# Kernel tuning notes

Hardware: AMD Instinct MI355X
Metric: run time of the kernel (lower is better)

The kernel has to match this reference:

```python
import jax, jax.numpy as jnp
import numpy as np

N_NODES = 100000
N_EDGES = 1000000
F_IN = 32       # CFG.feature_dim
H = 64          # CFG.hidden_dim
H2 = 2 * H      # L1 family: conv1 out = hidden_dim * 2
N_GRAPHS = 64


def gcn_conv(x, src, dst, deg_inv_sqrt, W, b, num_nodes):
    # PyG GCNConv: out = D^{-1/2} (A + I) D^{-1/2} (x @ W) + b
    h = x @ W  # [N, out]
    norm = (deg_inv_sqrt[src] * deg_inv_sqrt[dst])[:, None]  # [E+N, 1]
    msg = h[src] * norm
    return jax.ops.segment_sum(msg, dst, num_segments=num_nodes) + b


def setup_inputs() -> dict:
    key = jax.random.key(0)
    ks = jax.random.split(key, 10)
    x = jax.random.normal(ks[0], (N_NODES, F_IN), dtype=jnp.float32)
    edge_index = jax.random.randint(ks[1], (2, N_EDGES), 0, N_NODES, dtype=jnp.int64)
    batch = jnp.sort(jax.random.randint(ks[2], (N_NODES,), 0, N_GRAPHS, dtype=jnp.int64))
    def glorot(k, shape):
        lim = np.sqrt(6.0 / (shape[0] + shape[1]))
        return jax.random.uniform(k, shape, jnp.float32, -lim, lim)
    W1 = glorot(ks[3], (F_IN, H2))
    b1 = jnp.zeros((H2,), jnp.float32)
    W2 = glorot(ks[4], (H2, H))
    b2 = jnp.zeros((H,), jnp.float32)
    Wrt = glorot(ks[5], (H, H))
    brt = jnp.zeros((H,), jnp.float32)
    return {"x": x, "edge_index": edge_index, "batch": batch,
            "W1": W1, "b1": b1, "W2": W2, "b2": b2, "Wrt": Wrt, "brt": brt}


def reference(x, edge_index, batch, W1, b1, W2, b2, Wrt, brt):
    num_nodes = x.shape[0]
    loop = jnp.arange(num_nodes, dtype=edge_index.dtype)
    src = jnp.concatenate([edge_index[0], loop])  # add self-loops
    dst = jnp.concatenate([edge_index[1], loop])
    deg = jax.ops.segment_sum(jnp.ones_like(dst, dtype=x.dtype), dst, num_segments=num_nodes)
    deg_inv_sqrt = jnp.where(deg > 0, jax.lax.rsqrt(deg), 0.0)

    h = jax.nn.relu(gcn_conv(x, src, dst, deg_inv_sqrt, W1, b1, num_nodes))
    h = gcn_conv(h, src, dst, deg_inv_sqrt, W2, b2, num_nodes)
    h = h @ Wrt + brt  # L1 reverse transcriptase

    # global_mean_pool over batch segments
    sums = jax.ops.segment_sum(h, batch, num_segments=N_GRAPHS)
    counts = jax.ops.segment_sum(jnp.ones((num_nodes,), h.dtype), batch, num_segments=N_GRAPHS)
    pooled = sums / jnp.maximum(counts, 1.0)[:, None]

    activity_factor = 1.0  # age = 0 -> 1/(1+0)
    return pooled * activity_factor
```

## Files before the change

### kernel.cpp

```cpp
#include <hip/hip_runtime.h>

#define NN 100000
#define NE 1000000
#define FIN 32
#define H2 128
#define HH 64
#define NG 64
#define SLOT 16
#define OSLOT 48

#define BSH 9
#define BNODES 512
#define NB 196
#define CAPL 28
#define CAPB 6144
#define CHUNK 2048
#define NSPILL 4096

typedef __attribute__((ext_vector_type(8))) short short8;
typedef __attribute__((ext_vector_type(4))) float f32x4;
typedef __attribute__((ext_vector_type(2))) float f32x2;

__device__ __forceinline__ unsigned f2bf(float f) {
    unsigned u = __float_as_uint(f);
    return (u + 0x7FFFu + ((u >> 16) & 1u)) >> 16;
}
__device__ __forceinline__ float bf2f(unsigned u) {
    return __uint_as_float(u << 16);
}
__device__ __forceinline__ void acc8(float* a, float w, uint4 v) {
    a[0] = fmaf(w, bf2f(v.x & 0xFFFFu), a[0]);
    a[1] = fmaf(w, bf2f(v.x >> 16), a[1]);
    a[2] = fmaf(w, bf2f(v.y & 0xFFFFu), a[2]);
    a[3] = fmaf(w, bf2f(v.y >> 16), a[3]);
    a[4] = fmaf(w, bf2f(v.z & 0xFFFFu), a[4]);
    a[5] = fmaf(w, bf2f(v.z >> 16), a[5]);
    a[6] = fmaf(w, bf2f(v.w & 0xFFFFu), a[6]);
    a[7] = fmaf(w, bf2f(v.w >> 16), a[7]);
}
__device__ __forceinline__ void dec8(float* a, float w, uint2 v) {
    f32x2 p0 = __builtin_amdgcn_cvt_pk_f32_fp8((int)v.x, false);
    f32x2 p1 = __builtin_amdgcn_cvt_pk_f32_fp8((int)v.x, true);
    f32x2 p2 = __builtin_amdgcn_cvt_pk_f32_fp8((int)v.y, false);
    f32x2 p3 = __builtin_amdgcn_cvt_pk_f32_fp8((int)v.y, true);
    a[0] = fmaf(w, p0.x, a[0]); a[1] = fmaf(w, p0.y, a[1]);
    a[2] = fmaf(w, p1.x, a[2]); a[3] = fmaf(w, p1.y, a[3]);
    a[4] = fmaf(w, p2.x, a[4]); a[5] = fmaf(w, p2.y, a[5]);
    a[6] = fmaf(w, p3.x, a[6]); a[7] = fmaf(w, p3.y, a[7]);
}
__device__ __forceinline__ unsigned char f2fp8(float f) {
    return (unsigned char)(__builtin_amdgcn_cvt_pk_fp8_f32(f, f, 0, false) & 0xff);
}


__global__ void k_zero(int* __restrict__ p, int n) {
    int i = blockIdx.x * 256 + threadIdx.x;
    if (i < n) p[i] = 0;
}

__global__ void k_cvtx(const float* __restrict__ x, uint4* __restrict__ xb) {
    int i = blockIdx.x * 256 + threadIdx.x;
    if (i >= NN * FIN / 8) return;
    float4 a = ((const float4*)x)[2 * i];
    float4 b = ((const float4*)x)[2 * i + 1];
    uint4 r;
    r.x = f2bf(a.x) | (f2bf(a.y) << 16);
    r.y = f2bf(a.z) | (f2bf(a.w) << 16);
    r.z = f2bf(b.x) | (f2bf(b.y) << 16);
    r.w = f2bf(b.z) | (f2bf(b.w) << 16);
    xb[i] = r;
}

__global__ void k_fold(const float* __restrict__ W2, const float* __restrict__ Wrt,
                       const float* __restrict__ b2, const float* __restrict__ brt,
                       const float* __restrict__ W1,
                       unsigned short* __restrict__ w2t, float* __restrict__ brt2,
                       unsigned short* __restrict__ w1t) {
    int i = blockIdx.x * 256 + threadIdx.x;
    if (i < H2 * HH) {
        int r = i >> 6, c = i & 63;
        float acc = 0.f;
        for (int k = 0; k < HH; ++k) acc = fmaf(W2[r * HH + k], Wrt[k * HH + c], acc);
        w2t[c * H2 + r] = (unsigned short)f2bf(acc);
    } else if (i < H2 * HH + HH) {
        int c = i - H2 * HH;
        float acc = brt[c];
        for (int k = 0; k < HH; ++k) acc = fmaf(b2[k], Wrt[k * HH + c], acc);
        brt2[c] = acc;
    } else if (i < H2 * HH + HH + FIN * H2) {
        int j = i - (H2 * HH + HH);
        int k = j >> 7, c = j & 127;
        w1t[c * FIN + k] = (unsigned short)f2bf(W1[j]);
    }
}

__global__ __launch_bounds__(256) void k_bin(const int* __restrict__ ei,
                                             int* __restrict__ gcnt,
                                             unsigned* __restrict__ gbuf,
                                             int* __restrict__ gspillc,
                                             int* __restrict__ gspill) {
    __shared__ int cur[NB];
    __shared__ int gbase[NB];
    __shared__ unsigned stage[NB * CAPL];
    for (int i = threadIdx.x; i < NB; i += 256) cur[i] = 0;
    __syncthreads();
    int e0 = blockIdx.x * CHUNK;
#pragma unroll
    for (int it = 0; it < CHUNK / 256; ++it) {
        int e = e0 + it * 256 + threadIdx.x;
        if (e < NE) {
            int d = ei[NE + e];
            int b = d >> BSH;
            unsigned u = ((unsigned)ei[e] << BSH) | (unsigned)(d & (BNODES - 1));
            int p = atomicAdd(&cur[b], 1);
            if (p < CAPL) stage[b * CAPL + p] = u;
            else {
                int q = atomicAdd(gspillc, 1);
                if (q < NSPILL) { gspill[2 * q] = b; gspill[2 * q + 1] = (int)u; }
            }
        }
    }
    __syncthreads();
    if (threadIdx.x < NB) {
        int len = min(cur[threadIdx.x], CAPL);
        gbase[threadIdx.x] = len ? atomicAdd(&gcnt[threadIdx.x], len) : 0;
    }
    __syncthreads();
    int wid = threadIdx.x >> 6, lane = threadIdx.x & 63;
    for (int b = wid; b < NB; b += 4) {
        int len = min(cur[b], CAPL);
        if (len == 0) continue;
        int base = gbase[b];
        if (base + len > CAPB) len = max(0, CAPB - base);
        if (lane < len)
            gbuf[(size_t)b * CAPB + base + lane] = stage[b * CAPL + lane];
    }
}

__global__ __launch_bounds__(512) void k_build(const unsigned* __restrict__ gbuf,
                                               const int* __restrict__ gcnt,
                                               const int* __restrict__ gspillc,
                                               const int* __restrict__ gspill,
                                               int* __restrict__ esrc,
                                               int* __restrict__ ovf,
                                               int* __restrict__ fill) {
    __shared__ int cnt[BNODES];
    __shared__ int slots[BNODES * SLOT];
    for (int i = threadIdx.x; i < BNODES; i += 512) cnt[i] = 0;
    __syncthreads();
    int b = blockIdx.x;
    int len = min(gcnt[b], CAPB);
    const unsigned* buf = gbuf + (size_t)b * CAPB;
    for (int i = threadIdx.x; i < len; i += 512) {
        unsigned u = buf[i];
        int ln = u & (BNODES - 1);
        int src = (int)(u >> BSH);
        int p = atomicAdd(&cnt[ln], 1);
        if (p < SLOT) slots[ln * SLOT + p] = src;
        else if (p < SLOT + OSLOT)
            ovf[(size_t)(b * BNODES + ln) * OSLOT + (p - SLOT)] = src;
    }
    int ns = min(*gspillc, NSPILL);
    for (int i = threadIdx.x; i < ns; i += 512) {
        if (gspill[2 * i] == b) {
            unsigned u = (unsigned)gspill[2 * i + 1];
            int ln = u & (BNODES - 1);
            int src = (int)(u >> BSH);
            int p = atomicAdd(&cnt[ln], 1);
            if (p < SLOT) slots[ln * SLOT + p] = src;
            else if (p < SLOT + OSLOT)
                ovf[(size_t)(b * BNODES + ln) * OSLOT + (p - SLOT)] = src;
        }
    }
    __syncthreads();
    int nbase = b * BNODES;
    int nvalid = min(BNODES, NN - nbase);
    if (nvalid <= 0) return;
    for (int i = threadIdx.x; i < nvalid; i += 512) fill[nbase + i] = cnt[i];
    int nwords = nvalid * SLOT / 4;
    int4* d4 = (int4*)(esrc + (size_t)nbase * SLOT);
    const int4* s4 = (const int4*)slots;
    for (int i = threadIdx.x; i < nwords; i += 512) d4[i] = s4[i];
}

__global__ void k_node(const int* __restrict__ cnt, const int* __restrict__ bat,
                       float* __restrict__ dis, int* __restrict__ counts) {
    int n = blockIdx.x * 256 + threadIdx.x;
    int lane = threadIdx.x & 63;
    if (n < NN) dis[n] = rsqrtf((float)(cnt[n] + 1));
    int g = (n < NN) ? bat[n] : -1;
    int gprev = __shfl_up(g, 1, 64);
    bool head = (lane == 0) || (g != gprev);
    unsigned long long hm = __ballot(head && (n < NN));
    int gnext = __shfl_down(g, 1, 64);
    bool tail = (n < NN) && ((lane == 63) || (gnext != g));
    if (tail) {
        unsigned long long below =
            (lane == 63) ? ~0ull : ((1ull << (lane + 1)) - 1ull);
        int start = 63 - __clzll(hm & below);
        atomicAdd(&counts[g], lane - start + 1);
    }
}

__global__ void k_pack(const int* __restrict__ cnt, const float* __restrict__ dis,
                       int* __restrict__ esrc, int* __restrict__ ovf) {
    int i = blockIdx.x * 256 + threadIdx.x;
    if (i >= NN * 64) return;
    int n = i >> 6, p = i & 63;
    int c = cnt[n];
    if (p < SLOT) {
        if (p >= min(c, SLOT)) return;
        int s = esrc[n * SLOT + p];
        esrc[n * SLOT + p] = (int)(((unsigned)s << 15) | (f2bf(dis[s]) & 0x7FFFu));
    } else {
        int q = p - SLOT;
        if (q >= min(c - SLOT, OSLOT)) return;
        int s = ovf[n * OSLOT + q];
        ovf[n * OSLOT + q] = (int)(((unsigned)s << 15) | (f2bf(dis[s]) & 0x7FFFu));
    }
}

__global__ __launch_bounds__(256, 4) void k_aggx(
    const uint4* __restrict__ xb4, const float* __restrict__ dis,
    const int* __restrict__ cnt, const int* __restrict__ esrc,
    const int* __restrict__ ovf, uint4* __restrict__ aggx4) {
    int idx = blockIdx.x * 256 + threadIdx.x;
    int n = idx >> 2, t = idx & 3;
    if (n >= NN) return;
    float dn = dis[n];
    float a[8];
    {
        uint4 xv = xb4[n * 4 + t];
        float s = dn * dn;
        a[0] = s * bf2f(xv.x & 0xFFFFu); a[1] = s * bf2f(xv.x >> 16);
        a[2] = s * bf2f(xv.y & 0xFFFFu); a[3] = s * bf2f(xv.y >> 16);
        a[4] = s * bf2f(xv.z & 0xFFFFu); a[5] = s * bf2f(xv.z >> 16);
        a[6] = s * bf2f(xv.w & 0xFFFFu); a[7] = s * bf2f(xv.w >> 16);
    }
    int c = cnt[n];
    int c1 = min(c, SLOT);
    if (c1 > 0) {
        const int4* rp = (const int4*)(esrc + (size_t)n * SLOT);
        int4 i0 = rp[0], i1 = rp[1], i2 = rp[2], i3 = rp[3];
        int ej[16] = {i0.x, i0.y, i0.z, i0.w, i1.x, i1.y, i1.z, i1.w,
                      i2.x, i2.y, i2.z, i2.w, i3.x, i3.y, i3.z, i3.w};
        int e0 = i0.x;
#pragma unroll
        for (int j = 0; j < 16; ++j) {
            int e = (j < c1) ? ej[j] : e0;
            int s = (int)((unsigned)e >> 15);
            float w = (j < c1) ? bf2f(e & 0x7FFF) * dn : 0.f;
            acc8(a, w, xb4[(size_t)s * 4 + t]);
        }
    }
    if (c > SLOT) {
        int cov = min(c - SLOT, OSLOT);
        const int* orow = ovf + (size_t)n * OSLOT;
        for (int p = 0; p < cov; ++p) {
            int e = orow[p];
            int s = (int)((unsigned)e >> 15);
            acc8(a, bf2f(e & 0x7FFF) * dn, xb4[(size_t)s * 4 + t]);
        }
    }
    uint4 r;
    r.x = f2bf(a[0]) | (f2bf(a[1]) << 16);
    r.y = f2bf(a[2]) | (f2bf(a[3]) << 16);
    r.z = f2bf(a[4]) | (f2bf(a[5]) << 16);
    r.w = f2bf(a[6]) | (f2bf(a[7]) << 16);
    aggx4[n * 4 + t] = r;
}

__global__ __launch_bounds__(256) void k_mlpm(
    const unsigned short* __restrict__ aggxg, const unsigned short* __restrict__ w1tg,
    const unsigned short* __restrict__ w2tg, const float* __restrict__ b1,
    unsigned char* __restrict__ y) {
    __shared__ unsigned short w1t[H2 * FIN];
    __shared__ unsigned short w2t[HH * H2];
    __shared__ float b1s[H2];
    __shared__ float h1s[4][16 * 132];
    for (int i = threadIdx.x; i < FIN * H2 / 8; i += 256)
        ((uint4*)w1t)[i] = ((const uint4*)w1tg)[i];
    for (int i = threadIdx.x; i < HH * H2 / 8; i += 256)
        ((uint4*)w2t)[i] = ((const uint4*)w2tg)[i];
    if (threadIdx.x < H2) b1s[threadIdx.x] = b1[threadIdx.x];
    __syncthreads();
    int wid = threadIdx.x >> 6, l = threadIdx.x & 63;
    int base = (blockIdx.x * 4 + wid) * 16;
    if (base >= NN) return;
    int lr = l & 15, lk = l >> 4;
    float* h1w = h1s[wid];
    const f32x4 zero = {0.f, 0.f, 0.f, 0.f};

    short8 a1 = ((const short8*)aggxg)[(base + lr) * 4 + lk];
#pragma unroll
    for (int ct = 0; ct < 8; ++ct) {
        short8 bf = *(const short8*)&w1t[(ct * 16 + lr) * FIN + lk * 8];
        f32x4 c = __builtin_amdgcn_mfma_f32_16x16x32_bf16(a1, bf, zero, 0, 0, 0);
        float bv = b1s[ct * 16 + lr];
#pragma unroll
        for (int q = 0; q < 4; ++q)
            h1w[(lk * 4 + q) * 132 + ct * 16 + lr] = fmaxf(c[q] + bv, 0.f);
    }

    f32x4 acc0 = zero, acc1 = zero, acc2 = zero, acc3 = zero;
#pragma unroll
    for (int kt = 0; kt < 4; ++kt) {
        const float* ap = &h1w[lr * 132 + kt * 32 + lk * 8];
        float4 alo = *(const float4*)ap;
        float4 ahi = *(const float4*)(ap + 4);
        short8 af;
        af[0] = (short)f2bf(alo.x); af[1] = (short)f2bf(alo.y);
        af[2] = (short)f2bf(alo.z); af[3] = (short)f2bf(alo.w);
        af[4] = (short)f2bf(ahi.x); af[5] = (short)f2bf(ahi.y);
        af[6] = (short)f2bf(ahi.z); af[7] = (short)f2bf(ahi.w);
        const unsigned short* wb = &w2t[lr * H2 + kt * 32 + lk * 8];
        short8 b0 = *(const short8*)(wb);
        short8 b1f = *(const short8*)(wb + 16 * H2);
        short8 b2f = *(const short8*)(wb + 32 * H2);
        short8 b3f = *(const short8*)(wb + 48 * H2);
        acc0 = __builtin_amdgcn_mfma_f32_16x16x32_bf16(af, b0, acc0, 0, 0, 0);
        acc1 = __builtin_amdgcn_mfma_f32_16x16x32_bf16(af, b1f, acc1, 0, 0, 0);
        acc2 = __builtin_amdgcn_mfma_f32_16x16x32_bf16(af, b2f, acc2, 0, 0, 0);
        acc3 = __builtin_amdgcn_mfma_f32_16x16x32_bf16(af, b3f, acc3, 0, 0, 0);
    }
    unsigned char* ybs = (unsigned char*)h1w;
#pragma unroll
    for (int q = 0; q < 4; ++q) {
        int r = lk * 4 + q;
        ybs[r * 64 + lr +  0] = f2fp8(acc0[q]);
        ybs[r * 64 + lr + 16] = f2fp8(acc1[q]);
        ybs[r * 64 + lr + 32] = f2fp8(acc2[q]);
        ybs[r * 64 + lr + 48] = f2fp8(acc3[q]);
    }
    ((uint4*)(y + (size_t)base * 64))[l] = ((const uint4*)ybs)[l];
}

__global__ __launch_bounds__(256, 4) void k_l2g(
    const uint2* __restrict__ y2, const float* __restrict__ dis,
    const int* __restrict__ cnt, const int* __restrict__ esrc,
    const int* __restrict__ ovf, const float* __restrict__ brt2,
    const int* __restrict__ bat, float* __restrict__ pool) {
    __shared__ float hred[32][HH];
    __shared__ int gids[32];
    int idx = blockIdx.x * 256 + threadIdx.x;
    int n = idx >> 3;
    int t = threadIdx.x & 7;
    int ni = threadIdx.x >> 3;
    float dn = dis[n];
    float a[8];
    {
        float4 blo = ((const float4*)brt2)[t * 2];
        float4 bhi = ((const float4*)brt2)[t * 2 + 1];
        a[0] = blo.x; a[1] = blo.y; a[2] = blo.z; a[3] = blo.w;
        a[4] = bhi.x; a[5] = bhi.y; a[6] = bhi.z; a[7] = bhi.w;
        dec8(a, dn * dn, y2[(size_t)n * 8 + t]);
    }
    int c = cnt[n];
    int c1 = min(c, SLOT);
    if (c1 > 0) {
        const int4* rp = (const int4*)(esrc + (size_t)n * SLOT);
        int4 i0 = rp[0], i1 = rp[1], i2 = rp[2], i3 = rp[3];
        int ej[16] = {i0.x, i0.y, i0.z, i0.w, i1.x, i1.y, i1.z, i1.w,
                      i2.x, i2.y, i2.z, i2.w, i3.x, i3.y, i3.z, i3.w};
        int e0 = i0.x;
#pragma unroll
        for (int j = 0; j < 16; ++j) {
            int e = (j < c1) ? ej[j] : e0;
            int s = (int)((unsigned)e >> 15);
            float w = (j < c1) ? bf2f(e & 0x7FFF) * dn : 0.f;
            dec8(a, w, y2[(size_t)s * 8 + t]);
        }
    }
    if (c > SLOT) {
        int cov = min(c - SLOT, OSLOT);
        const int* orow = ovf + (size_t)n * OSLOT;
        for (int p = 0; p < cov; ++p) {
            int e = orow[p];
            int s = (int)((unsigned)e >> 15);
            dec8(a, bf2f(e & 0x7FFF) * dn, y2[(size_t)s * 8 + t]);
        }
    }
    ((float4*)&hred[ni][t * 8])[0] = make_float4(a[0], a[1], a[2], a[3]);
    ((float4*)&hred[ni][t * 8])[1] = make_float4(a[4], a[5], a[6], a[7]);
    if (t == 0) gids[ni] = bat[n];
    __syncthreads();
    if (threadIdx.x < HH) {
        int f = threadIdx.x;
        int cg = gids[0];
        float s = 0.f;
        for (int j = 0; j < 32; ++j) {
            int g = gids[j];
            if (g != cg) { atomicAdd(&pool[cg * HH + f], s); s = 0.f; cg = g; }
            s += hred[j][f];
        }
        atomicAdd(&pool[cg * HH + f], s);
    }
}

__global__ void k_final(const float* __restrict__ pool, const int* __restrict__ counts,
                        float* __restrict__ out) {
    int i = blockIdx.x * 256 + threadIdx.x;
    if (i < NG * HH) {
        int g = i >> 6;
        out[i] = pool[i] / fmaxf((float)counts[g], 1.0f);
    }
}


extern "C" void kernel_launch(void* const* d_in, const int* in_sizes, int n_in,
                              void* d_out, int out_size, void* d_ws, size_t ws_size,
                              hipStream_t stream) {
    const float* x   = (const float*)d_in[0];
    const int*   ei  = (const int*)d_in[1];
    const int*   bat = (const int*)d_in[2];
    const float* W1  = (const float*)d_in[3];
    const float* b1  = (const float*)d_in[4];
    const float* W2  = (const float*)d_in[5];
    const float* b2  = (const float*)d_in[6];
    const float* Wrt = (const float*)d_in[7];
    const float* brt = (const float*)d_in[8];
    float* out = (float*)d_out;

    int* ws = (int*)d_ws;
    int* fill    = ws;
    int* counts  = ws + NN;
    float* pool  = (float*)(ws + NN + NG);
    int* gcnt    = ws + NN + NG + NG * HH;
    int* gspillc = gcnt + 256;
    const int ZN = NN + NG + NG * HH + 256 + 64;
    int* gspill  = ws + ZN;
    float* dis   = (float*)(gspill + 2 * NSPILL);
    int* esrc    = (int*)dis + NN;
    int* ovf     = esrc + (size_t)NN * SLOT;
    unsigned* gbuf = (unsigned*)(ovf + (size_t)NN * OSLOT);
    unsigned* xb   = (unsigned*)(gbuf + (size_t)NB * CAPB);
    unsigned* aggx = xb + NN * 16;
    unsigned char* yb = (unsigned char*)(aggx + NN * 16);
    unsigned short* w1t = (unsigned short*)(yb + (size_t)NN * 64);
    unsigned short* w2t = w1t + FIN * H2;
    float* brt2 = (float*)(w2t + H2 * HH);

    k_zero<<<(ZN + 255) / 256, 256, 0, stream>>>(ws, ZN);
    k_cvtx<<<(NN * FIN / 8 + 255) / 256, 256, 0, stream>>>(x, (uint4*)xb);
    k_fold<<<(H2 * HH + HH + FIN * H2 + 255) / 256, 256, 0, stream>>>(
        W2, Wrt, b2, brt, W1, w2t, brt2, w1t);
    k_bin<<<(NE + CHUNK - 1) / CHUNK, 256, 0, stream>>>(ei, gcnt, gbuf, gspillc, gspill);
    k_build<<<NB, 512, 0, stream>>>(gbuf, gcnt, gspillc, gspill, esrc, ovf, fill);
    k_node<<<(NN + 255) / 256, 256, 0, stream>>>(fill, bat, dis, counts);
    k_pack<<<(NN * 64 + 255) / 256, 256, 0, stream>>>(fill, dis, esrc, ovf);
    k_aggx<<<(NN * 4 + 255) / 256, 256, 0, stream>>>(
        (const uint4*)xb, dis, fill, esrc, ovf, (uint4*)aggx);
    k_mlpm<<<(NN + 63) / 64, 256, 0, stream>>>(
        (const unsigned short*)aggx, w1t, w2t, b1, yb);
    k_l2g<<<NN * 8 / 256, 256, 0, stream>>>(
        (const uint2*)yb, dis, fill, esrc, ovf, brt2, bat, pool);
    k_final<<<(NG * HH + 255) / 256, 256, 0, stream>>>(pool, counts, out);
}
```

Measured before the change: 120.7 us.

## Store input features as fp8 and merge setup kernels into one launch

The bf16 copy of x is replaced by an fp8 copy, which halves the bytes fetched per neighbor in the layer-one gather. Aggregation decodes it with the hardware fp8 conversion instructions. The zero, convert and weight-fold kernels are merged into a single setup kernel, removing two launches. The cost is lower input precision, which could push the result past the accuracy tolerance.

```diff
diff --git a/kernel.cpp b/kernel.cpp
--- a/kernel.cpp
+++ b/kernel.cpp
@@ -16,6 +16,7 @@
 #define CAPB 6144
 #define CHUNK 2048
 #define NSPILL 4096
+#define ZN (NN + NG + NG * HH + 256 + 64)
 
 typedef __attribute__((ext_vector_type(8))) short short8;
 typedef __attribute__((ext_vector_type(4))) float f32x4;
@@ -27,16 +28,6 @@
 }
 __device__ __forceinline__ float bf2f(unsigned u) {
     return __uint_as_float(u << 16);
-}
-__device__ __forceinline__ void acc8(float* a, float w, uint4 v) {
-    a[0] = fmaf(w, bf2f(v.x & 0xFFFFu), a[0]);
-    a[1] = fmaf(w, bf2f(v.x >> 16), a[1]);
-    a[2] = fmaf(w, bf2f(v.y & 0xFFFFu), a[2]);
-    a[3] = fmaf(w, bf2f(v.y >> 16), a[3]);
-    a[4] = fmaf(w, bf2f(v.z & 0xFFFFu), a[4]);
-    a[5] = fmaf(w, bf2f(v.z >> 16), a[5]);
-    a[6] = fmaf(w, bf2f(v.w & 0xFFFFu), a[6]);
-    a[7] = fmaf(w, bf2f(v.w >> 16), a[7]);
 }
 __device__ __forceinline__ void dec8(float* a, float w, uint2 v) {
     f32x2 p0 = __builtin_amdgcn_cvt_pk_f32_fp8((int)v.x, false);
@@ -52,31 +43,23 @@
     return (unsigned char)(__builtin_amdgcn_cvt_pk_fp8_f32(f, f, 0, false) & 0xff);
 }
 
-
-__global__ void k_zero(int* __restrict__ p, int n) {
+__global__ void k_setup(const float* __restrict__ x, const float* __restrict__ W1,
+                        const float* __restrict__ W2, const float* __restrict__ Wrt,
+                        const float* __restrict__ b2, const float* __restrict__ brt,
+                        int* __restrict__ zws, uint2* __restrict__ xb8,
+                        unsigned short* __restrict__ w2t, float* __restrict__ brt2,
+                        unsigned short* __restrict__ w1t) {
     int i = blockIdx.x * 256 + threadIdx.x;
-    if (i < n) p[i] = 0;
-}
-
-__global__ void k_cvtx(const float* __restrict__ x, uint4* __restrict__ xb) {
-    int i = blockIdx.x * 256 + threadIdx.x;
-    if (i >= NN * FIN / 8) return;
-    float4 a = ((const float4*)x)[2 * i];
-    float4 b = ((const float4*)x)[2 * i + 1];
-    uint4 r;
-    r.x = f2bf(a.x) | (f2bf(a.y) << 16);
-    r.y = f2bf(a.z) | (f2bf(a.w) << 16);
-    r.z = f2bf(b.x) | (f2bf(b.y) << 16);
-    r.w = f2bf(b.z) | (f2bf(b.w) << 16);
-    xb[i] = r;
-}
-
-__global__ void k_fold(const float* __restrict__ W2, const float* __restrict__ Wrt,
-                       const float* __restrict__ b2, const float* __restrict__ brt,
-                       const float* __restrict__ W1,
-                       unsigned short* __restrict__ w2t, float* __restrict__ brt2,
-                       unsigned short* __restrict__ w1t) {
-    int i = blockIdx.x * 256 + threadIdx.x;
+    if (i < ZN) zws[i] = 0;
+    if (i < NN * FIN / 8) {
+        float4 a = ((const float4*)x)[2 * i];
+        float4 b = ((const float4*)x)[2 * i + 1];
+        unsigned u0 = __builtin_amdgcn_cvt_pk_fp8_f32(a.x, a.y, 0, false);
+        u0 = __builtin_amdgcn_cvt_pk_fp8_f32(a.z, a.w, u0, true);
+        unsigned u1 = __builtin_amdgcn_cvt_pk_fp8_f32(b.x, b.y, 0, false);
+        u1 = __builtin_amdgcn_cvt_pk_fp8_f32(b.z, b.w, u1, true);
+        xb8[i] = make_uint2(u0, u1);
+    }
     if (i < H2 * HH) {
         int r = i >> 6, c = i & 63;
         float acc = 0.f;
@@ -221,22 +204,15 @@
 }
 
 __global__ __launch_bounds__(256, 4) void k_aggx(
-    const uint4* __restrict__ xb4, const float* __restrict__ dis,
+    const uint2* __restrict__ xb8, const float* __restrict__ dis,
     const int* __restrict__ cnt, const int* __restrict__ esrc,
     const int* __restrict__ ovf, uint4* __restrict__ aggx4) {
     int idx = blockIdx.x * 256 + threadIdx.x;
     int n = idx >> 2, t = idx & 3;
     if (n >= NN) return;
     float dn = dis[n];
-    float a[8];
-    {
-        uint4 xv = xb4[n * 4 + t];
-        float s = dn * dn;
-        a[0] = s * bf2f(xv.x & 0xFFFFu); a[1] = s * bf2f(xv.x >> 16);
-        a[2] = s * bf2f(xv.y & 0xFFFFu); a[3] = s * bf2f(xv.y >> 16);
-        a[4] = s * bf2f(xv.z & 0xFFFFu); a[5] = s * bf2f(xv.z >> 16);
-        a[6] = s * bf2f(xv.w & 0xFFFFu); a[7] = s * bf2f(xv.w >> 16);
-    }
+    float a[8] = {0.f, 0.f, 0.f, 0.f, 0.f, 0.f, 0.f, 0.f};
+    dec8(a, dn * dn, xb8[n * 4 + t]);
     int c = cnt[n];
     int c1 = min(c, SLOT);
     if (c1 > 0) {
@@ -250,7 +226,7 @@
             int e = (j < c1) ? ej[j] : e0;
             int s = (int)((unsigned)e >> 15);
             float w = (j < c1) ? bf2f(e & 0x7FFF) * dn : 0.f;
-            acc8(a, w, xb4[(size_t)s * 4 + t]);
+            dec8(a, w, xb8[(size_t)s * 4 + t]);
         }
     }
     if (c > SLOT) {
@@ -259,7 +235,7 @@
         for (int p = 0; p < cov; ++p) {
             int e = orow[p];
             int s = (int)((unsigned)e >> 15);
-            acc8(a, bf2f(e & 0x7FFF) * dn, xb4[(size_t)s * 4 + t]);
+            dec8(a, bf2f(e & 0x7FFF) * dn, xb8[(size_t)s * 4 + t]);
         }
     }
     uint4 r;
@@ -427,29 +403,26 @@
     float* pool  = (float*)(ws + NN + NG);
     int* gcnt    = ws + NN + NG + NG * HH;
     int* gspillc = gcnt + 256;
-    const int ZN = NN + NG + NG * HH + 256 + 64;
     int* gspill  = ws + ZN;
     float* dis   = (float*)(gspill + 2 * NSPILL);
     int* esrc    = (int*)dis + NN;
     int* ovf     = esrc + (size_t)NN * SLOT;
     unsigned* gbuf = (unsigned*)(ovf + (size_t)NN * OSLOT);
-    unsigned* xb   = (unsigned*)(gbuf + (size_t)NB * CAPB);
-    unsigned* aggx = xb + NN * 16;
+    uint2* xb8     = (uint2*)(gbuf + (size_t)NB * CAPB);
+    unsigned* aggx = (unsigned*)xb8 + NN * 8;
     unsigned char* yb = (unsigned char*)(aggx + NN * 16);
     unsigned short* w1t = (unsigned short*)(yb + (size_t)NN * 64);
     unsigned short* w2t = w1t + FIN * H2;
     float* brt2 = (float*)(w2t + H2 * HH);
 
-    k_zero<<<(ZN + 255) / 256, 256, 0, stream>>>(ws, ZN);
-    k_cvtx<<<(NN * FIN / 8 + 255) / 256, 256, 0, stream>>>(x, (uint4*)xb);
-    k_fold<<<(H2 * HH + HH + FIN * H2 + 255) / 256, 256, 0, stream>>>(
-        W2, Wrt, b2, brt, W1, w2t, brt2, w1t);
+    k_setup<<<(NN * FIN / 8 + 255) / 256, 256, 0, stream>>>(
+        x, W1, W2, Wrt, b2, brt, ws, xb8, w2t, brt2, w1t);
     k_bin<<<(NE + CHUNK - 1) / CHUNK, 256, 0, stream>>>(ei, gcnt, gbuf, gspillc, gspill);
     k_build<<<NB, 512, 0, stream>>>(gbuf, gcnt, gspillc, gspill, esrc, ovf, fill);
     k_node<<<(NN + 255) / 256, 256, 0, stream>>>(fill, bat, dis, counts);
     k_pack<<<(NN * 64 + 255) / 256, 256, 0, stream>>>(fill, dis, esrc, ovf);
     k_aggx<<<(NN * 4 + 255) / 256, 256, 0, stream>>>(
-        (const uint4*)xb, dis, fill, esrc, ovf, (uint4*)aggx);
+        xb8, dis, fill, esrc, ovf, (uint4*)aggx);
     k_mlpm<<<(NN + 63) / 64, 256, 0, stream>>>(
         (const unsigned short*)aggx, w1t, w2t, b1, yb);
     k_l2g<<<NN * 8 / 256, 256, 0, stream>>>(
```

After: 109.9 us. -8.9%, faster.
